# Optimization experiments

Hardware: AMD Instinct MI355X
Metric: run time of the kernel (lower is better)

## Reference

```python
import jax, jax.numpy as jnp
import numpy as np

DIM = 96
WIN = (5, 6, 5)          # (wd, wh, ww)
SHAPE = (2, 96, 40, 48, 40)  # B, C, D, H, W


def _rel_pos_index(win):
    """Swin-3D relative position index, [N, N] int, N = wd*wh*ww."""
    wd, wh, ww = win
    coords = np.stack(np.meshgrid(np.arange(wd), np.arange(wh), np.arange(ww), indexing='ij'))
    cf = coords.reshape(3, -1)                       # [3, N]
    rel = (cf[:, :, None] - cf[:, None, :]).transpose(1, 2, 0).astype(np.int64)  # [N,N,3]
    rel[..., 0] += wd - 1
    rel[..., 1] += wh - 1
    rel[..., 2] += ww - 1
    rel[..., 0] *= (2 * wh - 1) * (2 * ww - 1)
    rel[..., 1] *= (2 * ww - 1)
    return rel.sum(-1)                               # [N, N]


def _ln(x, g, b):
    m = x.mean(-1, keepdims=True)
    v = x.var(-1, keepdims=True)
    return (x - m) * jax.lax.rsqrt(v + 1e-5) * g + b


def _win_partition(x, win):
    # x: [B, D, H, W, C] -> [B*nW, wd*wh*ww, C]
    B, D, H, W, C = x.shape
    wd, wh, ww = win
    x = x.reshape(B, D // wd, wd, H // wh, wh, W // ww, ww, C)
    x = x.transpose(0, 1, 3, 5, 2, 4, 6, 7)
    return x.reshape(-1, wd * wh * ww, C)


def _win_reverse(xw, win, B, D, H, W):
    wd, wh, ww = win
    C = xw.shape[-1]
    x = xw.reshape(B, D // wd, H // wh, W // ww, wd, wh, ww, C)
    x = x.transpose(0, 1, 4, 2, 5, 3, 6, 7)
    return x.reshape(B, D, H, W, C)


def setup_inputs() -> dict:
    key = jax.random.key(0)
    ks = jax.random.split(key, 16)
    B, C, D, H, W = SHAPE
    hid = 4 * C
    n_bias = (2 * WIN[0] - 1) * (2 * WIN[1] - 1) * (2 * WIN[2] - 1)
    f32 = jnp.float32
    return {
        'I_m': jax.random.normal(ks[0], (B, C, D, H, W), f32),
        'I_f': jax.random.normal(ks[1], (B, C, D, H, W), f32),
        'ln1q_g': jnp.ones((C,), f32), 'ln1q_b': jnp.zeros((C,), f32),
        'ln1kv_g': jnp.ones((C,), f32), 'ln1kv_b': jnp.zeros((C,), f32),
        'wq': jax.random.normal(ks[2], (C, C), f32) * 0.02,
        'bq': jnp.zeros((C,), f32),
        'wkv': jax.random.normal(ks[3], (C, 2 * C), f32) * 0.02,
        'bkv': jnp.zeros((2 * C,), f32),
        'wproj': jax.random.normal(ks[4], (C, C), f32) * 0.02,
        'bproj': jnp.zeros((C,), f32),
        'rel_bias': jax.random.normal(ks[5], (n_bias, 1), f32) * 0.02,
        'ln2_g': jnp.ones((C,), f32), 'ln2_b': jnp.zeros((C,), f32),
        'mlp_w1': jax.random.normal(ks[6], (C, hid), f32) * 0.02,
        'mlp_b1': jnp.zeros((hid,), f32),
        'mlp_w2': jax.random.normal(ks[7], (hid, C), f32) * 0.02,
        'mlp_b2': jnp.zeros((C,), f32),
        'conv_w': jax.random.normal(ks[8], (3, C, 3, 3, 3), f32) * 1e-5,  # RegistrationHead Normal(0,1e-5)
        'conv_b': jnp.zeros((3,), f32),
    }


def reference(I_m, I_f, ln1q_g, ln1q_b, ln1kv_g, ln1kv_b, wq, bq, wkv, bkv,
              wproj, bproj, rel_bias, ln2_g, ln2_b, mlp_w1, mlp_b1, mlp_w2,
              mlp_b2, conv_w, conv_b):
    B, C, D, H, W = I_m.shape
    N = WIN[0] * WIN[1] * WIN[2]
    idx = jnp.asarray(_rel_pos_index(WIN))           # [N, N] constant

    # channels-last tokens
    x = I_m.transpose(0, 2, 3, 4, 1)                 # [B, D, H, W, C]
    y = I_f.transpose(0, 2, 3, 4, 1)
    shortcut = x

    xw = _win_partition(_ln(x, ln1q_g, ln1q_b), WIN)   # [BnW, N, C]
    yw = _win_partition(_ln(y, ln1kv_g, ln1kv_b), WIN)

    q = xw @ wq + bq                                  # [BnW, N, C]
    kv = yw @ wkv + bkv
    k, v = kv[..., :C], kv[..., C:]

    scale = C ** -0.5                                 # num_heads = 1
    bias = rel_bias[idx].squeeze(-1)                  # [N, N]
    attn = jnp.einsum('wnc,wmc->wnm', q, k) * scale + bias
    attn = jax.nn.softmax(attn, axis=-1)
    out = jnp.einsum('wnm,wmc->wnc', attn, v) @ wproj + bproj

    x = shortcut + _win_reverse(out, WIN, B, D, H, W)
    h = _ln(x, ln2_g, ln2_b)
    x = x + (jax.nn.gelu(h @ mlp_w1 + mlp_b1) @ mlp_w2 + mlp_b2)

    feat = x.transpose(0, 4, 1, 2, 3)                 # [B, C, D, H, W]
    flow = jax.lax.conv_general_dilated(
        feat, conv_w, window_strides=(1, 1, 1), padding=[(1, 1)] * 3,
        dimension_numbers=('NCDHW', 'OIDHW', 'NCDHW'))
    return flow + conv_b[None, :, None, None, None]
```

## Files before the change

kernel.cpp:

```cpp
#include <hip/hip_runtime.h>
#include <math.h>


static constexpr int NTOK = 153600;
static constexpr float SCALE = 0.10206207261596575f;

typedef __bf16 bf16_t;
typedef __bf16 bf16x8 __attribute__((ext_vector_type(8)));
typedef float f32x4 __attribute__((ext_vector_type(4)));

__device__ __forceinline__ int tok_index(int b, int d, int h, int w) {
    int d0 = d / 5, wd = d % 5;
    int h0 = h / 6, wh = h % 6;
    int w0 = w / 5, ww = w % 5;
    int win = ((b * 8 + d0) * 8 + h0) * 8 + w0;
    return win * 150 + (wd * 6 + wh) * 5 + ww;
}

__device__ __forceinline__ float gelu_f(float u) {
    float u2 = u * u;
    float arg = u * fmaf(0.0713549f, u2, 1.5957691f);
    float e = __expf(arg);
    float r = __builtin_amdgcn_rcpf(e + 1.f);
    return fmaf(-u, r, u);
}

__global__ __launch_bounds__(256) void k_prep_weights(
    const float* __restrict__ wq, const float* __restrict__ wkv,
    const float* __restrict__ w1, const float* __restrict__ w2,
    const float* __restrict__ wproj, const float* __restrict__ relb,
    const float* __restrict__ cw,
    bf16_t* wqT, bf16_t* wkvT, bf16_t* w1T, bf16_t* w2T, bf16_t* wpjT,
    float* bias_mat, float* cwT)
{
    int i = blockIdx.x * 256 + threadIdx.x;
    if (i < 9216)  wqT[i]  = (bf16_t)wq[(i % 96) * 96 + i / 96];
    if (i < 18432) wkvT[i] = (bf16_t)wkv[(i % 96) * 192 + i / 96];
    if (i < 36864) w1T[i]  = (bf16_t)w1[(i % 96) * 384 + i / 96];
    if (i < 36864) w2T[i]  = (bf16_t)w2[(i % 384) * 96 + i / 384];
    if (i < 9216)  wpjT[i] = (bf16_t)wproj[(i % 96) * 96 + i / 96];
    if (i < 25600) {
        int row = i / 160, col = i % 160;
        float v;
        if (col >= 150) v = -1e30f;
        else if (row >= 150) v = 0.f;
        else {
            int wd1 = row / 30, rh1 = row % 30, wh1 = rh1 / 5, ww1 = rh1 % 5;
            int wd2 = col / 30, rh2 = col % 30, wh2 = rh2 / 5, ww2 = rh2 % 5;
            int idx = (wd1 - wd2 + 4) * 99 + (wh1 - wh2 + 5) * 9 + (ww1 - ww2 + 4);
            v = relb[idx];
        }
        bias_mat[i] = v;
    }
    if (i < 7776) {
        int kk = i / 288, rem = i % 288;
        int oc = rem / 96, ci = rem % 96;
        cwT[i] = cw[oc * 2592 + ci * 27 + kk];
    }
}

__global__ __launch_bounds__(256) void k_ln_transpose(
    const float* __restrict__ Im, const float* __restrict__ If,
    const float* __restrict__ g1q, const float* __restrict__ b1q,
    const float* __restrict__ g1k, const float* __restrict__ b1k,
    bf16_t* __restrict__ xln, bf16_t* __restrict__ yln,
    float* __restrict__ x2s)
{
    __shared__ float tile[40 * 97];
    __shared__ float mean_s[40], rstd_s[40];
    int blk = blockIdx.x;
    int b = blk / (40 * 48);
    int rem = blk % (40 * 48);
    int d = rem / 48, h = rem % 48;
    int tid = threadIdx.x;

    for (int pass = 0; pass < 2; ++pass) {
        const float* src = pass ? If : Im;
        const float* gg = pass ? g1k : g1q;
        const float* bb = pass ? b1k : b1q;
        bf16_t* dst = pass ? yln : xln;

        for (int i = tid; i < 96 * 40; i += 256) {
            int c = i / 40, w = i % 40;
            tile[w * 97 + c] = src[(size_t)(b * 96 + c) * 76800 + d * 1920 + h * 40 + w];
        }
        __syncthreads();
        if (tid < 40) {
            float s = 0.f, s2 = 0.f;
            for (int c = 0; c < 96; ++c) {
                float v = tile[tid * 97 + c];
                s += v; s2 += v * v;
            }
            float m = s * (1.f / 96.f);
            float var = s2 * (1.f / 96.f) - m * m;
            mean_s[tid] = m;
            rstd_s[tid] = rsqrtf(var + 1e-5f);
        }
        __syncthreads();
        for (int i = tid; i < 40 * 96; i += 256) {
            int w = i / 96, c = i % 96;
            int tok = tok_index(b, d, h, w);
            float raw = tile[w * 97 + c];
            float v = (raw - mean_s[w]) * rstd_s[w] * gg[c] + bb[c];
            dst[(size_t)tok * 96 + c] = (bf16_t)v;
            if (pass == 0) x2s[(size_t)tok * 96 + c] = raw;
        }
        __syncthreads();
    }
}

__global__ __launch_bounds__(256) void k_proj_mfma(
    const bf16_t* __restrict__ X, const bf16_t* __restrict__ WT,
    const float* __restrict__ bias, int N,
    bf16_t* __restrict__ outA, bf16_t* __restrict__ vT)
{
    extern __shared__ bf16_t sm[];
    bf16_t* xs  = sm;
    bf16_t* wsh = sm + 64 * 104;
    int tid = threadIdx.x;
    int t0 = blockIdx.x * 64;

    const uint4* xg = (const uint4*)(X + (size_t)t0 * 96);
    uint4* xsv = (uint4*)xs;
    for (int i = tid; i < 768; i += 256) {
        int row = i / 12, c16 = i % 12;
        xsv[row * 13 + c16] = xg[i];
    }
    const uint4* wg = (const uint4*)WT;
    uint4* wsv = (uint4*)wsh;
    for (int i = tid; i < N * 12; i += 256) {
        int row = i / 12, c16 = i % 12;
        wsv[row * 13 + c16] = wg[i];
    }
    __syncthreads();

    int w = tid >> 6, l = tid & 63;
    int lm = l & 15, lk = (l >> 4) * 8;
    int m0 = w * 16;
    bf16x8 a[3];
#pragma unroll
    for (int kk = 0; kk < 3; ++kk)
        a[kk] = *(const bf16x8*)(xs + (m0 + lm) * 104 + kk * 32 + lk);

    int trow[4], twin[4], tm[4];
#pragma unroll
    for (int r = 0; r < 4; ++r) {
        int t = t0 + m0 + (l >> 4) * 4 + r;
        trow[r] = t; twin[r] = t / 150; tm[r] = t - twin[r] * 150;
    }

    int ntiles = N >> 4;
    for (int ti = 0; ti < ntiles; ++ti) {
        int n0 = ti * 16;
        f32x4 c = {0.f, 0.f, 0.f, 0.f};
        const bf16_t* wp = wsh + (size_t)(n0 + lm) * 104 + lk;
        c = __builtin_amdgcn_mfma_f32_16x16x32_bf16(a[0], *(const bf16x8*)(wp), c, 0, 0, 0);
        c = __builtin_amdgcn_mfma_f32_16x16x32_bf16(a[1], *(const bf16x8*)(wp + 32), c, 0, 0, 0);
        c = __builtin_amdgcn_mfma_f32_16x16x32_bf16(a[2], *(const bf16x8*)(wp + 64), c, 0, 0, 0);
        int n = n0 + lm;
        float bs = bias[n];
        if (n < 96) {
#pragma unroll
            for (int r = 0; r < 4; ++r)
                outA[(size_t)trow[r] * 96 + n] = (bf16_t)(c[r] + bs);
        } else {
            int cc = n - 96;
#pragma unroll
            for (int r = 0; r < 4; ++r)
                vT[((size_t)twin[r] * 96 + cc) * 160 + tm[r]] = (bf16_t)(c[r] + bs);
        }
    }
}

__global__ __launch_bounds__(384) void k_attn_mfma(
    const bf16_t* __restrict__ qb, const bf16_t* __restrict__ kb,
    const bf16_t* __restrict__ vT, const bf16_t* __restrict__ wpjT,
    const float* __restrict__ bias_mat, const float* __restrict__ bproj,
    float* __restrict__ x2)
{
    __shared__ __align__(16) bf16_t kls[160 * 104];
    __shared__ __align__(16) bf16_t pls_all[6 * 16 * 164];
    int win = blockIdx.x;
    int tid = threadIdx.x;
    int wv = tid >> 6, l = tid & 63;
    int lm = l & 15, lq = l >> 4, lk8 = lq * 8;
    size_t wbase = (size_t)win * 150 * 96;
    size_t vbase = (size_t)win * 96 * 160;
    bf16_t* pls = pls_all + wv * 16 * 164;

    {
        const uint4* src = (const uint4*)(kb + wbase);
        for (int i = tid; i < 1800; i += 384) {
            int row = i / 12, c = i % 12;
            *(uint4*)(kls + row * 104 + c * 8) = src[i];
        }
        uint4 z = {0, 0, 0, 0};
        for (int i = tid; i < 130; i += 384) {
            int row = 150 + i / 13, c = i % 13;
            *(uint4*)(kls + row * 104 + c * 8) = z;
        }
    }
    __syncthreads();

    for (int ti = wv; ti < 10; ti += 6) {
        int r0 = ti * 16;

        bf16x8 aq[3];
#pragma unroll
        for (int kk = 0; kk < 3; ++kk)
            aq[kk] = *(const bf16x8*)(qb + wbase + (size_t)(r0 + lm) * 96 + kk * 32 + lk8);

        f32x4 s[10];
#pragma unroll
        for (int nt = 0; nt < 10; ++nt) {
            f32x4 acc = {0.f, 0.f, 0.f, 0.f};
            const bf16_t* kp = kls + (nt * 16 + lm) * 104 + lk8;
            acc = __builtin_amdgcn_mfma_f32_16x16x32_bf16(aq[0], *(const bf16x8*)(kp), acc, 0, 0, 0);
            acc = __builtin_amdgcn_mfma_f32_16x16x32_bf16(aq[1], *(const bf16x8*)(kp + 32), acc, 0, 0, 0);
            acc = __builtin_amdgcn_mfma_f32_16x16x32_bf16(aq[2], *(const bf16x8*)(kp + 64), acc, 0, 0, 0);
            s[nt] = acc;
        }

#pragma unroll
        for (int r = 0; r < 4; ++r) {
            int grow = r0 + lq * 4 + r;
            float rowmax = -3.0e38f;
#pragma unroll
            for (int nt = 0; nt < 10; ++nt) {
                float bv = bias_mat[grow * 160 + nt * 16 + lm];
                float v = fmaf(s[nt][r], SCALE, bv);
                s[nt][r] = v;
                rowmax = fmaxf(rowmax, v);
            }
            rowmax = fmaxf(rowmax, __shfl_xor(rowmax, 1));
            rowmax = fmaxf(rowmax, __shfl_xor(rowmax, 2));
            rowmax = fmaxf(rowmax, __shfl_xor(rowmax, 4));
            rowmax = fmaxf(rowmax, __shfl_xor(rowmax, 8));
            float ssum = 0.f;
#pragma unroll
            for (int nt = 0; nt < 10; ++nt) {
                float e = __expf(s[nt][r] - rowmax);
                s[nt][r] = e;
                ssum += e;
            }
            ssum += __shfl_xor(ssum, 1);
            ssum += __shfl_xor(ssum, 2);
            ssum += __shfl_xor(ssum, 4);
            ssum += __shfl_xor(ssum, 8);
            float inv = 1.f / ssum;
            int lrow = lq * 4 + r;
#pragma unroll
            for (int nt = 0; nt < 10; ++nt)
                pls[lrow * 164 + nt * 16 + lm] = (bf16_t)(s[nt][r] * inv);
        }

        f32x4 o[6];
#pragma unroll
        for (int ct = 0; ct < 6; ++ct) o[ct] = (f32x4){0.f, 0.f, 0.f, 0.f};
#pragma unroll
        for (int kf = 0; kf < 5; ++kf) {
            bf16x8 ap = *(const bf16x8*)(pls + lm * 164 + kf * 32 + lk8);
#pragma unroll
            for (int ct = 0; ct < 6; ++ct) {
                const bf16_t* vp = vT + vbase + (size_t)(ct * 16 + lm) * 160 + kf * 32 + lk8;
                o[ct] = __builtin_amdgcn_mfma_f32_16x16x32_bf16(ap, *(const bf16x8*)(vp), o[ct], 0, 0, 0);
            }
        }

#pragma unroll
        for (int ct = 0; ct < 6; ++ct)
#pragma unroll
            for (int r = 0; r < 4; ++r)
                pls[(lq * 4 + r) * 104 + ct * 16 + lm] = (bf16_t)o[ct][r];

        bf16x8 ao[3];
#pragma unroll
        for (int kk = 0; kk < 3; ++kk)
            ao[kk] = *(const bf16x8*)(pls + lm * 104 + kk * 32 + lk8);
        f32x4 pj[6];
#pragma unroll
        for (int ct = 0; ct < 6; ++ct) {
            f32x4 acc = {0.f, 0.f, 0.f, 0.f};
            const bf16_t* wp = wpjT + (size_t)(ct * 16 + lm) * 96 + lk8;
            acc = __builtin_amdgcn_mfma_f32_16x16x32_bf16(ao[0], *(const bf16x8*)(wp), acc, 0, 0, 0);
            acc = __builtin_amdgcn_mfma_f32_16x16x32_bf16(ao[1], *(const bf16x8*)(wp + 32), acc, 0, 0, 0);
            acc = __builtin_amdgcn_mfma_f32_16x16x32_bf16(ao[2], *(const bf16x8*)(wp + 64), acc, 0, 0, 0);
            pj[ct] = acc;
        }
#pragma unroll
        for (int r = 0; r < 4; ++r) {
            int gr = r0 + lq * 4 + r;
            if (gr < 150) {
                size_t t = (size_t)win * 150 + gr;
#pragma unroll
                for (int ct = 0; ct < 6; ++ct) {
                    int c = ct * 16 + lm;
                    size_t off = t * 96 + c;
                    x2[off] = x2[off] + pj[ct][r] + bproj[c];
                }
            }
        }
    }
}

__global__ __launch_bounds__(256, 3) void k_mlp_mfma(
    const float* __restrict__ x2,
    const float* __restrict__ g2, const float* __restrict__ b2,
    const bf16_t* __restrict__ w1T, const float* __restrict__ b1,
    const bf16_t* __restrict__ w2T, const float* __restrict__ b2v,
    bf16_t* __restrict__ xc)
{
    __shared__ __align__(16) bf16_t xs[128 * 104];
    __shared__ __align__(16) bf16_t hs[4 * 32 * 104];

    int tid = threadIdx.x;
    int t0 = blockIdx.x * 128;

    {
        int t = tid >> 1, p = tid & 1;
        float xr[48];
        const float4* xg = (const float4*)(x2 + (size_t)(t0 + t) * 96 + p * 48);
#pragma unroll
        for (int j4 = 0; j4 < 12; ++j4) {
            float4 v = xg[j4];
            xr[j4 * 4 + 0] = v.x; xr[j4 * 4 + 1] = v.y;
            xr[j4 * 4 + 2] = v.z; xr[j4 * 4 + 3] = v.w;
        }
        float s = 0.f, s2 = 0.f;
#pragma unroll
        for (int j = 0; j < 48; ++j) { s += xr[j]; s2 += xr[j] * xr[j]; }
        s += __shfl_xor(s, 1);
        s2 += __shfl_xor(s2, 1);
        float m = s * (1.f / 96.f);
        float var = s2 * (1.f / 96.f) - m * m;
        float rstd = rsqrtf(var + 1e-5f);

        const float4* gg = (const float4*)(g2 + p * 48);
        const float4* bb = (const float4*)(b2 + p * 48);
        bf16_t tmp[48];
#pragma unroll
        for (int j4 = 0; j4 < 12; ++j4) {
            float4 g = gg[j4], bv = bb[j4];
            tmp[j4 * 4 + 0] = (bf16_t)((xr[j4 * 4 + 0] - m) * rstd * g.x + bv.x);
            tmp[j4 * 4 + 1] = (bf16_t)((xr[j4 * 4 + 1] - m) * rstd * g.y + bv.y);
            tmp[j4 * 4 + 2] = (bf16_t)((xr[j4 * 4 + 2] - m) * rstd * g.z + bv.z);
            tmp[j4 * 4 + 3] = (bf16_t)((xr[j4 * 4 + 3] - m) * rstd * g.w + bv.w);
        }
        uint4* dst = (uint4*)(xs + t * 104 + p * 48);
        const uint4* src = (const uint4*)tmp;
#pragma unroll
        for (int j = 0; j < 6; ++j) dst[j] = src[j];
    }

    int w = tid >> 6, l = tid & 63;
    int lm = l & 15, lq = l >> 4, lk = lq * 8;
    int m0 = w * 32;
    bf16_t* hw = hs + w * 32 * 104;

    bf16x8 a[2][3];
#pragma unroll
    for (int mt = 0; mt < 2; ++mt)
#pragma unroll
        for (int kk = 0; kk < 3; ++kk)
            a[mt][kk] = *(const bf16x8*)(xs + (m0 + mt * 16 + lm) * 104 + kk * 32 + lk);

    f32x4 acc2[2][6];
#pragma unroll
    for (int mt = 0; mt < 2; ++mt)
#pragma unroll
        for (int i = 0; i < 6; ++i) acc2[mt][i] = (f32x4){0.f, 0.f, 0.f, 0.f};

#pragma unroll
    for (int cc = 0; cc < 4; ++cc) {
#pragma unroll
        for (int ti = 0; ti < 6; ++ti) {
            int n = cc * 96 + ti * 16 + lm;
            const bf16_t* wp = w1T + (size_t)n * 96 + lk;
            bf16x8 w0 = *(const bf16x8*)(wp);
            bf16x8 w1v = *(const bf16x8*)(wp + 32);
            bf16x8 w2v = *(const bf16x8*)(wp + 64);
            float bs = b1[n];
#pragma unroll
            for (int mt = 0; mt < 2; ++mt) {
                f32x4 c1 = {0.f, 0.f, 0.f, 0.f};
                c1 = __builtin_amdgcn_mfma_f32_16x16x32_bf16(a[mt][0], w0, c1, 0, 0, 0);
                c1 = __builtin_amdgcn_mfma_f32_16x16x32_bf16(a[mt][1], w1v, c1, 0, 0, 0);
                c1 = __builtin_amdgcn_mfma_f32_16x16x32_bf16(a[mt][2], w2v, c1, 0, 0, 0);
#pragma unroll
                for (int r = 0; r < 4; ++r)
                    hw[(mt * 16 + lq * 4 + r) * 104 + ti * 16 + lm] =
                        (bf16_t)gelu_f(c1[r] + bs);
            }
        }

        bf16x8 ha[2][3];
#pragma unroll
        for (int mt = 0; mt < 2; ++mt)
#pragma unroll
            for (int kk = 0; kk < 3; ++kk)
                ha[mt][kk] = *(const bf16x8*)(hw + (mt * 16 + lm) * 104 + kk * 32 + lk);
#pragma unroll
        for (int ti = 0; ti < 6; ++ti) {
            const bf16_t* wp = w2T + (size_t)(ti * 16 + lm) * 384 + cc * 96 + lk;
            bf16x8 v0 = *(const bf16x8*)(wp);
            bf16x8 v1 = *(const bf16x8*)(wp + 32);
            bf16x8 v2 = *(const bf16x8*)(wp + 64);
#pragma unroll
            for (int mt = 0; mt < 2; ++mt) {
                acc2[mt][ti] = __builtin_amdgcn_mfma_f32_16x16x32_bf16(ha[mt][0], v0, acc2[mt][ti], 0, 0, 0);
                acc2[mt][ti] = __builtin_amdgcn_mfma_f32_16x16x32_bf16(ha[mt][1], v1, acc2[mt][ti], 0, 0, 0);
                acc2[mt][ti] = __builtin_amdgcn_mfma_f32_16x16x32_bf16(ha[mt][2], v2, acc2[mt][ti], 0, 0, 0);
            }
        }
    }

#pragma unroll
    for (int mt = 0; mt < 2; ++mt) {
        int srow[4];
#pragma unroll
        for (int r = 0; r < 4; ++r) {
            int t = t0 + m0 + mt * 16 + lq * 4 + r;
            int win = t / 150, nn = t - win * 150;
            int b = win >> 9, d0 = (win >> 6) & 7, h0 = (win >> 3) & 7, w0 = win & 7;
            int wd = nn / 30, rem = nn % 30, wh = rem / 5, ww = rem % 5;
            srow[r] = ((b * 40 + d0 * 5 + wd) * 48 + h0 * 6 + wh) * 40 + w0 * 5 + ww;
        }
#pragma unroll
        for (int ti = 0; ti < 6; ++ti) {
            int n = ti * 16 + lm;
            float bs = b2v[n];
#pragma unroll
            for (int r = 0; r < 4; ++r) {
                int t = t0 + m0 + mt * 16 + lq * 4 + r;
                size_t o = (size_t)t * 96 + n;
                xc[(size_t)srow[r] * 96 + n] = (bf16_t)(x2[o] + acc2[mt][ti][r] + bs);
            }
        }
    }
}

__global__ __launch_bounds__(256) void k_conv(
    const bf16_t* __restrict__ xc, const float* __restrict__ cwT,
    const float* __restrict__ cb, float* __restrict__ out)
{
    __shared__ float wl[7776];
    int tid = threadIdx.x;
    for (int i = tid; i < 7776; i += 256) wl[i] = cwT[i];
    __syncthreads();

    int gid = blockIdx.x * 256 + tid;
    int s = gid >> 2, p = gid & 3;
    int b = s / 76800, r = s % 76800;
    int d = r / 1920, h = (r / 40) % 48, w = r % 40;
    float a0 = 0.f, a1 = 0.f, a2 = 0.f;

    for (int dd = 0; dd < 3; ++dd) {
        int d2 = d + dd - 1;
        if ((unsigned)d2 >= 40u) continue;
        for (int hh = 0; hh < 3; ++hh) {
            int h2 = h + hh - 1;
            if ((unsigned)h2 >= 48u) continue;
            for (int ww = 0; ww < 3; ++ww) {
                int w2 = w + ww - 1;
                if ((unsigned)w2 >= 40u) continue;
                int kk = (dd * 3 + hh) * 3 + ww;
                const bf16x8* xp = (const bf16x8*)
                    (xc + ((size_t)((b * 40 + d2) * 48 + h2) * 40 + w2) * 96 + p * 24);
                const float* wk = wl + kk * 288 + p * 24;
#pragma unroll
                for (int c8 = 0; c8 < 3; ++c8) {
                    bf16x8 xv = xp[c8];
                    float x0 = (float)xv[0], x1 = (float)xv[1];
                    float x2v = (float)xv[2], x3 = (float)xv[3];
                    float x4 = (float)xv[4], x5 = (float)xv[5];
                    float x6 = (float)xv[6], x7 = (float)xv[7];
                    float4 wa0 = *(const float4*)(wk + c8 * 8);
                    float4 wb0 = *(const float4*)(wk + c8 * 8 + 4);
                    float4 wa1 = *(const float4*)(wk + 96 + c8 * 8);
                    float4 wb1 = *(const float4*)(wk + 96 + c8 * 8 + 4);
                    float4 wa2 = *(const float4*)(wk + 192 + c8 * 8);
                    float4 wb2 = *(const float4*)(wk + 192 + c8 * 8 + 4);
                    a0 += x0 * wa0.x + x1 * wa0.y + x2v * wa0.z + x3 * wa0.w
                        + x4 * wb0.x + x5 * wb0.y + x6 * wb0.z + x7 * wb0.w;
                    a1 += x0 * wa1.x + x1 * wa1.y + x2v * wa1.z + x3 * wa1.w
                        + x4 * wb1.x + x5 * wb1.y + x6 * wb1.z + x7 * wb1.w;
                    a2 += x0 * wa2.x + x1 * wa2.y + x2v * wa2.z + x3 * wa2.w
                        + x4 * wb2.x + x5 * wb2.y + x6 * wb2.z + x7 * wb2.w;
                }
            }
        }
    }
    a0 += __shfl_xor(a0, 1); a0 += __shfl_xor(a0, 2);
    a1 += __shfl_xor(a1, 1); a1 += __shfl_xor(a1, 2);
    a2 += __shfl_xor(a2, 1); a2 += __shfl_xor(a2, 2);
    float av = (p == 0) ? a0 : ((p == 1) ? a1 : a2);
    if (p < 3)
        out[(size_t)(b * 3 + p) * 76800 + r] = av + cb[p];
}

extern "C" void kernel_launch(void* const* d_in, const int* in_sizes, int n_in,
                              void* d_out, int out_size, void* d_ws, size_t ws_size,
                              hipStream_t stream)
{
    (void)in_sizes; (void)n_in; (void)out_size;

    const float* Im  = (const float*)d_in[0];
    const float* If  = (const float*)d_in[1];
    const float* g1q = (const float*)d_in[2];
    const float* b1q = (const float*)d_in[3];
    const float* g1k = (const float*)d_in[4];
    const float* b1k = (const float*)d_in[5];
    const float* wq  = (const float*)d_in[6];
    const float* bq  = (const float*)d_in[7];
    const float* wkv = (const float*)d_in[8];
    const float* bkv = (const float*)d_in[9];
    const float* wpj = (const float*)d_in[10];
    const float* bpj = (const float*)d_in[11];
    const float* rb  = (const float*)d_in[12];
    const float* g2  = (const float*)d_in[13];
    const float* b2  = (const float*)d_in[14];
    const float* w1  = (const float*)d_in[15];
    const float* b1  = (const float*)d_in[16];
    const float* w2  = (const float*)d_in[17];
    const float* b2v = (const float*)d_in[18];
    const float* cw  = (const float*)d_in[19];
    const float* cb  = (const float*)d_in[20];
    float* out = (float*)d_out;

    size_t U = (size_t)NTOK * 96;
    if (ws_size < 4 * U * sizeof(float)) return;
    float* ws = (float*)d_ws;
    bf16_t* xlnb = (bf16_t*)ws;
    bf16_t* ylnb = (bf16_t*)(ws + U / 2);
    bf16_t* qb   = (bf16_t*)(ws + U);
    bf16_t* kb   = (bf16_t*)(ws + 3 * U / 2);
    bf16_t* vT   = (bf16_t*)(ws + 2 * U);
    float*  wtail = ws + 2 * U + (1024 * 96 * 160) / 2;
    bf16_t* wqT  = (bf16_t*)wtail;
    bf16_t* wkvT = wqT + 9216;
    bf16_t* w1T  = wkvT + 18432;
    bf16_t* w2T  = w1T + 36864;
    bf16_t* wpjT = w2T + 36864;
    float*  bias_mat = (float*)(wpjT + 9216 + 2);
    float*  cwT  = bias_mat + 25600;
    float*  x2f  = ws + 3 * U;
    bf16_t* xc   = (bf16_t*)ws;

    k_prep_weights<<<144, 256, 0, stream>>>(wq, wkv, w1, w2, wpj, rb, cw,
                                            wqT, wkvT, w1T, w2T, wpjT,
                                            bias_mat, cwT);
    k_ln_transpose<<<3840, 256, 0, stream>>>(Im, If, g1q, b1q, g1k, b1k,
                                             xlnb, ylnb, x2f);
    size_t shm_q  = (size_t)(64 * 104 + 96 * 104) * sizeof(bf16_t);
    size_t shm_kv = (size_t)(64 * 104 + 192 * 104) * sizeof(bf16_t);
    k_proj_mfma<<<2400, 256, shm_q, stream>>>(xlnb, wqT, bq, 96, qb, nullptr);
    k_proj_mfma<<<2400, 256, shm_kv, stream>>>(ylnb, wkvT, bkv, 192, kb, vT);
    k_attn_mfma<<<1024, 384, 0, stream>>>(qb, kb, vT, wpjT, bias_mat, bpj, x2f);
    k_mlp_mfma<<<1200, 256, 0, stream>>>(x2f, g2, b2, w1T, b1, w2T, b2v, xc);
    k_conv<<<2400, 256, 0, stream>>>(xc, cwT, cb, out);
}
```

Baseline: 581.5 us.

## Split attention into per-wave row-tile tasks and defer residual add to MLP

```diff
diff --git a/kernel.cpp b/kernel.cpp
--- a/kernel.cpp
+++ b/kernel.cpp
@@ -172,132 +172,116 @@
     }
 }
 
-__global__ __launch_bounds__(384) void k_attn_mfma(
+__global__ __launch_bounds__(256, 4) void k_attn_mfma(
     const bf16_t* __restrict__ qb, const bf16_t* __restrict__ kb,
     const bf16_t* __restrict__ vT, const bf16_t* __restrict__ wpjT,
     const float* __restrict__ bias_mat, const float* __restrict__ bproj,
-    float* __restrict__ x2)
-{
-    __shared__ __align__(16) bf16_t kls[160 * 104];
-    __shared__ __align__(16) bf16_t pls_all[6 * 16 * 164];
-    int win = blockIdx.x;
+    bf16_t* __restrict__ aob)
+{
+    __shared__ __align__(16) bf16_t pls_all[4 * 16 * 164];
     int tid = threadIdx.x;
     int wv = tid >> 6, l = tid & 63;
+    int task = blockIdx.x * 4 + wv;
+    int win = task / 10, ti = task - win * 10;
     int lm = l & 15, lq = l >> 4, lk8 = lq * 8;
     size_t wbase = (size_t)win * 150 * 96;
     size_t vbase = (size_t)win * 96 * 160;
     bf16_t* pls = pls_all + wv * 16 * 164;
-
-    {
-        const uint4* src = (const uint4*)(kb + wbase);
-        for (int i = tid; i < 1800; i += 384) {
-            int row = i / 12, c = i % 12;
-            *(uint4*)(kls + row * 104 + c * 8) = src[i];
-        }
-        uint4 z = {0, 0, 0, 0};
-        for (int i = tid; i < 130; i += 384) {
-            int row = 150 + i / 13, c = i % 13;
-            *(uint4*)(kls + row * 104 + c * 8) = z;
-        }
-    }
-    __syncthreads();
-
-    for (int ti = wv; ti < 10; ti += 6) {
-        int r0 = ti * 16;
-
-        bf16x8 aq[3];
-#pragma unroll
-        for (int kk = 0; kk < 3; ++kk)
-            aq[kk] = *(const bf16x8*)(qb + wbase + (size_t)(r0 + lm) * 96 + kk * 32 + lk8);
-
-        f32x4 s[10];
+    int r0 = ti * 16;
+
+    bf16x8 aq[3];
+#pragma unroll
+    for (int kk = 0; kk < 3; ++kk)
+        aq[kk] = *(const bf16x8*)(qb + wbase + (size_t)(r0 + lm) * 96 + kk * 32 + lk8);
+
+    f32x4 s[10];
+#pragma unroll
+    for (int nt = 0; nt < 10; ++nt) {
+        int krow = nt * 16 + lm;
+        if (krow > 149) krow = 149;
+        f32x4 acc = {0.f, 0.f, 0.f, 0.f};
+        const bf16_t* kp = kb + wbase + (size_t)krow * 96 + lk8;
+        acc = __builtin_amdgcn_mfma_f32_16x16x32_bf16(aq[0], *(const bf16x8*)(kp), acc, 0, 0, 0);
+        acc = __builtin_amdgcn_mfma_f32_16x16x32_bf16(aq[1], *(const bf16x8*)(kp + 32), acc, 0, 0, 0);
+        acc = __builtin_amdgcn_mfma_f32_16x16x32_bf16(aq[2], *(const bf16x8*)(kp + 64), acc, 0, 0, 0);
+        s[nt] = acc;
+    }
+
+#pragma unroll
+    for (int r = 0; r < 4; ++r) {
+        int grow = r0 + lq * 4 + r;
+        float rowmax = -3.0e38f;
 #pragma unroll
         for (int nt = 0; nt < 10; ++nt) {
-            f32x4 acc = {0.f, 0.f, 0.f, 0.f};
-            const bf16_t* kp = kls + (nt * 16 + lm) * 104 + lk8;
-            acc = __builtin_amdgcn_mfma_f32_16x16x32_bf16(aq[0], *(const bf16x8*)(kp), acc, 0, 0, 0);
-            acc = __builtin_amdgcn_mfma_f32_16x16x32_bf16(aq[1], *(const bf16x8*)(kp + 32), acc, 0, 0, 0);
-            acc = __builtin_amdgcn_mfma_f32_16x16x32_bf16(aq[2], *(const bf16x8*)(kp + 64), acc, 0, 0, 0);
-            s[nt] = acc;
-        }
-
-#pragma unroll
-        for (int r = 0; r < 4; ++r) {
-            int grow = r0 + lq * 4 + r;
-            float rowmax = -3.0e38f;
-#pragma unroll
-            for (int nt = 0; nt < 10; ++nt) {
-                float bv = bias_mat[grow * 160 + nt * 16 + lm];
-                float v = fmaf(s[nt][r], SCALE, bv);
-                s[nt][r] = v;
-                rowmax = fmaxf(rowmax, v);
-            }
-            rowmax = fmaxf(rowmax, __shfl_xor(rowmax, 1));
-            rowmax = fmaxf(rowmax, __shfl_xor(rowmax, 2));
-            rowmax = fmaxf(rowmax, __shfl_xor(rowmax, 4));
-            rowmax = fmaxf(rowmax, __shfl_xor(rowmax, 8));
-            float ssum = 0.f;
-#pragma unroll
-            for (int nt = 0; nt < 10; ++nt) {
-                float e = __expf(s[nt][r] - rowmax);
-                s[nt][r] = e;
-                ssum += e;
-            }
-            ssum += __shfl_xor(ssum, 1);
-            ssum += __shfl_xor(ssum, 2);
-            ssum += __shfl_xor(ssum, 4);
-            ssum += __shfl_xor(ssum, 8);
-            float inv = 1.f / ssum;
-            int lrow = lq * 4 + r;
-#pragma unroll
-            for (int nt = 0; nt < 10; ++nt)
-                pls[lrow * 164 + nt * 16 + lm] = (bf16_t)(s[nt][r] * inv);
-        }
-
-        f32x4 o[6];
-#pragma unroll
-        for (int ct = 0; ct < 6; ++ct) o[ct] = (f32x4){0.f, 0.f, 0.f, 0.f};
-#pragma unroll
-        for (int kf = 0; kf < 5; ++kf) {
-            bf16x8 ap = *(const bf16x8*)(pls + lm * 164 + kf * 32 + lk8);
+            float bv = bias_mat[grow * 160 + nt * 16 + lm];
+            float v = fmaf(s[nt][r], SCALE, bv);
+            s[nt][r] = v;
+            rowmax = fmaxf(rowmax, v);
+        }
+        rowmax = fmaxf(rowmax, __shfl_xor(rowmax, 1));
+        rowmax = fmaxf(rowmax, __shfl_xor(rowmax, 2));
+        rowmax = fmaxf(rowmax, __shfl_xor(rowmax, 4));
+        rowmax = fmaxf(rowmax, __shfl_xor(rowmax, 8));
+        float ssum = 0.f;
+#pragma unroll
+        for (int nt = 0; nt < 10; ++nt) {
+            float e = __expf(s[nt][r] - rowmax);
+            s[nt][r] = e;
+            ssum += e;
+        }
+        ssum += __shfl_xor(ssum, 1);
+        ssum += __shfl_xor(ssum, 2);
+        ssum += __shfl_xor(ssum, 4);
+        ssum += __shfl_xor(ssum, 8);
+        float inv = 1.f / ssum;
+        int lrow = lq * 4 + r;
+#pragma unroll
+        for (int nt = 0; nt < 10; ++nt)
+            pls[lrow * 164 + nt * 16 + lm] = (bf16_t)(s[nt][r] * inv);
+    }
+
+    f32x4 o[6];
+#pragma unroll
+    for (int ct = 0; ct < 6; ++ct) o[ct] = (f32x4){0.f, 0.f, 0.f, 0.f};
+#pragma unroll
+    for (int kf = 0; kf < 5; ++kf) {
+        bf16x8 ap = *(const bf16x8*)(pls + lm * 164 + kf * 32 + lk8);
+#pragma unroll
+        for (int ct = 0; ct < 6; ++ct) {
+            const bf16_t* vp = vT + vbase + (size_t)(ct * 16 + lm) * 160 + kf * 32 + lk8;
+            o[ct] = __builtin_amdgcn_mfma_f32_16x16x32_bf16(ap, *(const bf16x8*)(vp), o[ct], 0, 0, 0);
+        }
+    }
+
+#pragma unroll
+    for (int ct = 0; ct < 6; ++ct)
+#pragma unroll
+        for (int r = 0; r < 4; ++r)
+            pls[(lq * 4 + r) * 104 + ct * 16 + lm] = (bf16_t)o[ct][r];
+
+    bf16x8 ao[3];
+#pragma unroll
+    for (int kk = 0; kk < 3; ++kk)
+        ao[kk] = *(const bf16x8*)(pls + lm * 104 + kk * 32 + lk8);
+    f32x4 pj[6];
+#pragma unroll
+    for (int ct = 0; ct < 6; ++ct) {
+        f32x4 acc = {0.f, 0.f, 0.f, 0.f};
+        const bf16_t* wp = wpjT + (size_t)(ct * 16 + lm) * 96 + lk8;
+        acc = __builtin_amdgcn_mfma_f32_16x16x32_bf16(ao[0], *(const bf16x8*)(wp), acc, 0, 0, 0);
+        acc = __builtin_amdgcn_mfma_f32_16x16x32_bf16(ao[1], *(const bf16x8*)(wp + 32), acc, 0, 0, 0);
+        acc = __builtin_amdgcn_mfma_f32_16x16x32_bf16(ao[2], *(const bf16x8*)(wp + 64), acc, 0, 0, 0);
+        pj[ct] = acc;
+    }
+#pragma unroll
+    for (int r = 0; r < 4; ++r) {
+        int gr = r0 + lq * 4 + r;
+        if (gr < 150) {
+            size_t t = (size_t)win * 150 + gr;
 #pragma unroll
             for (int ct = 0; ct < 6; ++ct) {
-                const bf16_t* vp = vT + vbase + (size_t)(ct * 16 + lm) * 160 + kf * 32 + lk8;
-                o[ct] = __builtin_amdgcn_mfma_f32_16x16x32_bf16(ap, *(const bf16x8*)(vp), o[ct], 0, 0, 0);
-            }
-        }
-
-#pragma unroll
-        for (int ct = 0; ct < 6; ++ct)
-#pragma unroll
-            for (int r = 0; r < 4; ++r)
-                pls[(lq * 4 + r) * 104 + ct * 16 + lm] = (bf16_t)o[ct][r];
-
-        bf16x8 ao[3];
-#pragma unroll
-        for (int kk = 0; kk < 3; ++kk)
-            ao[kk] = *(const bf16x8*)(pls + lm * 104 + kk * 32 + lk8);
-        f32x4 pj[6];
-#pragma unroll
-        for (int ct = 0; ct < 6; ++ct) {
-            f32x4 acc = {0.f, 0.f, 0.f, 0.f};
-            const bf16_t* wp = wpjT + (size_t)(ct * 16 + lm) * 96 + lk8;
-            acc = __builtin_amdgcn_mfma_f32_16x16x32_bf16(ao[0], *(const bf16x8*)(wp), acc, 0, 0, 0);
-            acc = __builtin_amdgcn_mfma_f32_16x16x32_bf16(ao[1], *(const bf16x8*)(wp + 32), acc, 0, 0, 0);
-            acc = __builtin_amdgcn_mfma_f32_16x16x32_bf16(ao[2], *(const bf16x8*)(wp + 64), acc, 0, 0, 0);
-            pj[ct] = acc;
-        }
-#pragma unroll
-        for (int r = 0; r < 4; ++r) {
-            int gr = r0 + lq * 4 + r;
-            if (gr < 150) {
-                size_t t = (size_t)win * 150 + gr;
-#pragma unroll
-                for (int ct = 0; ct < 6; ++ct) {
-                    int c = ct * 16 + lm;
-                    size_t off = t * 96 + c;
-                    x2[off] = x2[off] + pj[ct][r] + bproj[c];
-                }
+                int c = ct * 16 + lm;
+                aob[t * 96 + c] = (bf16_t)(pj[ct][r] + bproj[c]);
             }
         }
     }
@@ -305,6 +289,7 @@
 
 __global__ __launch_bounds__(256, 3) void k_mlp_mfma(
     const float* __restrict__ x2,
+    const bf16_t* __restrict__ aob,
     const float* __restrict__ g2, const float* __restrict__ b2,
     const bf16_t* __restrict__ w1T, const float* __restrict__ b1,
     const bf16_t* __restrict__ w2T, const float* __restrict__ b2v,
@@ -320,11 +305,19 @@
         int t = tid >> 1, p = tid & 1;
         float xr[48];
         const float4* xg = (const float4*)(x2 + (size_t)(t0 + t) * 96 + p * 48);
+        const bf16x8* ag = (const bf16x8*)(aob + (size_t)(t0 + t) * 96 + p * 48);
 #pragma unroll
         for (int j4 = 0; j4 < 12; ++j4) {
             float4 v = xg[j4];
             xr[j4 * 4 + 0] = v.x; xr[j4 * 4 + 1] = v.y;
             xr[j4 * 4 + 2] = v.z; xr[j4 * 4 + 3] = v.w;
+        }
+#pragma unroll
+        for (int j8 = 0; j8 < 6; ++j8) {
+            bf16x8 av = ag[j8];
+#pragma unroll
+            for (int e = 0; e < 8; ++e)
+                xr[j8 * 8 + e] += (float)av[e];
         }
         float s = 0.f, s2 = 0.f;
 #pragma unroll
@@ -433,7 +426,8 @@
             for (int r = 0; r < 4; ++r) {
                 int t = t0 + m0 + mt * 16 + lq * 4 + r;
                 size_t o = (size_t)t * 96 + n;
-                xc[(size_t)srow[r] * 96 + n] = (bf16_t)(x2[o] + acc2[mt][ti][r] + bs);
+                float base = x2[o] + (float)aob[o];
+                xc[(size_t)srow[r] * 96 + n] = (bf16_t)(base + acc2[mt][ti][r] + bs);
             }
         }
     }
@@ -544,7 +538,8 @@
     float*  bias_mat = (float*)(wpjT + 9216 + 2);
     float*  cwT  = bias_mat + 25600;
     float*  x2f  = ws + 3 * U;
-    bf16_t* xc   = (bf16_t*)ws;
+    bf16_t* aob  = (bf16_t*)ws;
+    bf16_t* xc   = (bf16_t*)(ws + U / 2);
 
     k_prep_weights<<<144, 256, 0, stream>>>(wq, wkv, w1, w2, wpj, rb, cw,
                                             wqT, wkvT, w1T, w2T, wpjT,
@@ -555,7 +550,7 @@
     size_t shm_kv = (size_t)(64 * 104 + 192 * 104) * sizeof(bf16_t);
     k_proj_mfma<<<2400, 256, shm_q, stream>>>(xlnb, wqT, bq, 96, qb, nullptr);
     k_proj_mfma<<<2400, 256, shm_kv, stream>>>(ylnb, wkvT, bkv, 192, kb, vT);
-    k_attn_mfma<<<1024, 384, 0, stream>>>(qb, kb, vT, wpjT, bias_mat, bpj, x2f);
-    k_mlp_mfma<<<1200, 256, 0, stream>>>(x2f, g2, b2, w1T, b1, w2T, b2v, xc);
+    k_attn_mfma<<<2560, 256, 0, stream>>>(qb, kb, vT, wpjT, bias_mat, bpj, aob);
+    k_mlp_mfma<<<1200, 256, 0, stream>>>(x2f, aob, g2, b2, w1T, b1, w2T, b2v, xc);
     k_conv<<<2400, 256, 0, stream>>>(xc, cwT, cb, out);
 }
```

Result: faster. 535.9 us (-7.8%).
